# Optimization experiments

Hardware: AMD Instinct MI355X
Metric: run time of the kernel (lower is better)

The kernel has to match this reference:

```python
import jax, jax.numpy as jnp
import numpy as np

EPS = 1e-12  # matches torch F.normalize default


def _l2norm_c(x):
    # normalize along channel dim (axis=1) of [B,C,H,W]
    n = jnp.sqrt(jnp.sum(x * x, axis=1, keepdims=True))
    return x / jnp.maximum(n, EPS)


def setup_inputs() -> dict:
    key = jax.random.key(0)
    ks = jax.random.split(key, 6)
    B, C, H, W = 2, 256, 64, 64
    return {
        "sv": jax.random.normal(ks[0], (B, 1, H, W), dtype=jnp.float32),
        "si": jax.random.normal(ks[1], (B, 1, H, W), dtype=jnp.float32),
        "sf": jax.random.normal(ks[2], (B, 1, H, W), dtype=jnp.float32),
        "dv": jax.random.normal(ks[3], (B, C, H, W), dtype=jnp.float32),
        "di": jax.random.normal(ks[4], (B, C, H, W), dtype=jnp.float32),
        "df": jax.random.normal(ks[5], (B, C, H, W), dtype=jnp.float32),
    }


def reference(sv, si, sf, dv, di, df):
    # keypoint score loss: L1(sf, max(sv, si))
    kp = jnp.mean(jnp.abs(sf - jnp.maximum(sv, si)))
    # descriptor loss: L1(df, (dv+di)/2)
    desc = jnp.mean(jnp.abs(df - (dv + di) * 0.5))
    # match loss (dense): normalize along C, full correlation volumes, L1
    a = _l2norm_c(dv)
    b = _l2norm_c(di)
    c = _l2norm_c(df)
    sim_ab = jnp.einsum('bchw,bcij->bhwij', a, b)  # [B,H,W,H,W]
    sim_ac = jnp.einsum('bchw,bcij->bhwij', a, c)
    match = jnp.mean(jnp.abs(sim_ac - sim_ab))
    return kp + desc + match
```

## Files before the change

### kernel.cpp

```cpp
#include <hip/hip_runtime.h>
#include <hip/hip_bf16.h>
#include <math.h>

#define BB 2
#define CC 256
#define CCP (CC + 2)
#define HWN 4096
#define PT 32
#define TM 128

typedef __attribute__((ext_vector_type(4))) int   intx4;
typedef __attribute__((ext_vector_type(8))) int   intx8;
typedef __attribute__((ext_vector_type(4))) float floatx4;

__device__ __forceinline__ unsigned short f2bf(float f) {
    union { float f; unsigned u; } v; v.f = f;
    unsigned r = v.u + 0x7FFF + ((v.u >> 16) & 1);
    return (unsigned short)(r >> 16);
}

__device__ __forceinline__ float bf2f(unsigned short h) {
    union { unsigned u; float f; } v; v.u = ((unsigned)h) << 16;
    return v.f;
}

__device__ __forceinline__ void load_lds16(const void* g, void* l) {
    __builtin_amdgcn_global_load_lds(
        (const __attribute__((address_space(1))) unsigned int*)g,
        (__attribute__((address_space(3))) unsigned int*)l, 16, 0, 0);
}

__global__ __launch_bounds__(1024) void prep_kernel(
    const float* __restrict__ sv, const float* __restrict__ si,
    const float* __restrict__ sf, const float* __restrict__ dv,
    const float* __restrict__ di, const float* __restrict__ df,
    unsigned char* __restrict__ Af8, unsigned char* __restrict__ Df8,
    float* __restrict__ pk, float* __restrict__ pd)
{
    __shared__ unsigned short lv[PT][CCP];
    __shared__ unsigned short li[PT][CCP];
    __shared__ unsigned short lf[PT][CCP];
    __shared__ float ssq[3][PT];
    __shared__ float inv[3][PT];
    __shared__ float sdesc;

    const int b   = blockIdx.x / (HWN / PT);
    const int p0  = (blockIdx.x % (HWN / PT)) * PT;
    const int tid = threadIdx.x;
    const int tp  = tid & (PT - 1);
    const int cs  = tid >> 5;

    if (tid < 3 * PT) ((float*)ssq)[tid] = 0.0f;
    if (tid == 0) sdesc = 0.0f;
    __syncthreads();

    float sqv = 0.f, sqi = 0.f, sqf = 0.f, descp = 0.f;
    const size_t base = (size_t)b * CC * HWN + p0 + tp;
    #pragma unroll
    for (int j = 0; j < 8; ++j) {
        const int c = cs * 8 + j;
        const size_t idx = base + (size_t)c * HWN;
        const float v = dv[idx], ii = di[idx], ff = df[idx];
        descp += fabsf(ff - 0.5f * (v + ii));
        sqv += v * v; sqi += ii * ii; sqf += ff * ff;
        lv[tp][c] = f2bf(v); li[tp][c] = f2bf(ii); lf[tp][c] = f2bf(ff);
    }
    sqv += __shfl_down(sqv, 32);
    sqi += __shfl_down(sqi, 32);
    sqf += __shfl_down(sqf, 32);
    if ((tid & 63) < 32) {
        atomicAdd(&ssq[0][tp], sqv);
        atomicAdd(&ssq[1][tp], sqi);
        atomicAdd(&ssq[2][tp], sqf);
    }

    #pragma unroll
    for (int off = 32; off > 0; off >>= 1) descp += __shfl_down(descp, off);
    if ((tid & 63) == 0) atomicAdd(&sdesc, descp);

    if (tid < 64) {
        float kpv = 0.f;
        if (tid < PT) {
            const size_t sidx = (size_t)b * HWN + p0 + tid;
            kpv = fabsf(sf[sidx] - fmaxf(sv[sidx], si[sidx]));
        }
        #pragma unroll
        for (int off = 32; off > 0; off >>= 1) kpv += __shfl_down(kpv, off);
        if (tid == 0) pk[blockIdx.x] = kpv;
    }
    __syncthreads();

    if (tid < 3 * PT) {
        const float s = ((float*)ssq)[tid];
        ((float*)inv)[tid] = 1.0f / fmaxf(sqrtf(s), 1e-12f);
    }
    __syncthreads();

    if (tid == 0) pd[blockIdx.x] = sdesc;

    int* Ao = (int*)(Af8 + ((size_t)b * HWN + p0) * CC);
    int* Do = (int*)(Df8 + ((size_t)b * HWN + p0) * CC);
    #pragma unroll
    for (int i = tid; i < PT * CC / 4; i += 1024) {
        const int p = i >> 6, c0 = (i & 63) * 4;
        const float ia = inv[0][p], ib = inv[1][p], ic = inv[2][p];
        float a0 = bf2f(lv[p][c0 + 0]) * ia, a1 = bf2f(lv[p][c0 + 1]) * ia;
        float a2 = bf2f(lv[p][c0 + 2]) * ia, a3 = bf2f(lv[p][c0 + 3]) * ia;
        float d0 = bf2f(lf[p][c0 + 0]) * ic - bf2f(li[p][c0 + 0]) * ib;
        float d1 = bf2f(lf[p][c0 + 1]) * ic - bf2f(li[p][c0 + 1]) * ib;
        float d2 = bf2f(lf[p][c0 + 2]) * ic - bf2f(li[p][c0 + 2]) * ib;
        float d3 = bf2f(lf[p][c0 + 3]) * ic - bf2f(li[p][c0 + 3]) * ib;
        int wa = __builtin_amdgcn_cvt_pk_fp8_f32(a0, a1, 0, false);
        wa     = __builtin_amdgcn_cvt_pk_fp8_f32(a2, a3, wa, true);
        int wd = __builtin_amdgcn_cvt_pk_fp8_f32(d0, d1, 0, false);
        wd     = __builtin_amdgcn_cvt_pk_fp8_f32(d2, d3, wd, true);
        Ao[i] = wa;
        Do[i] = wd;
    }
}

__global__ __launch_bounds__(256) void gemm_abs_kernel(
    const unsigned char* __restrict__ Af8,
    const unsigned char* __restrict__ Df8,
    float* __restrict__ pg)
{
    __shared__ unsigned char lA[TM * CC];
    __shared__ unsigned char lB[TM * CC];

    const int b    = blockIdx.z;
    const int bm   = blockIdx.x * TM;
    const int bn   = blockIdx.y * TM;
    const int tid  = threadIdx.x;
    const int wave = tid >> 6;
    const int lane = tid & 63;
    const int wr   = wave >> 1, wc = wave & 1;

    const unsigned char* Agb = Af8 + (size_t)b * HWN * CC + (size_t)bm * CC;
    const unsigned char* Dgb = Df8 + (size_t)b * HWN * CC + (size_t)bn * CC;

    #pragma unroll
    for (int i = 0; i < 8; ++i) {
        const int r0 = wave * 32 + i * 4;
        const int r  = r0 + (lane >> 4);
        const int cs = (lane & 15) ^ (r & 15);
        const size_t gof = (size_t)r * CC + cs * 16;
        load_lds16(Agb + gof, (char*)lA + r0 * CC);
        load_lds16(Dgb + gof, (char*)lB + r0 * CC);
    }
    __syncthreads();

    floatx4 accf[4][4];
    #pragma unroll
    for (int mi = 0; mi < 4; ++mi)
        #pragma unroll
        for (int ni = 0; ni < 4; ++ni)
            accf[mi][ni] = (floatx4){0.f, 0.f, 0.f, 0.f};

    #pragma unroll
    for (int ks = 0; ks < 2; ++ks) {
        const int cb = ks * 8 + (lane >> 4) * 2;
        intx8 a8[4], b8[4];
        #pragma unroll
        for (int mi = 0; mi < 4; ++mi) {
            const int m = wr * 64 + mi * 16 + (lane & 15);
            const char* pa = (const char*)lA + m * CC;
            intx4 lo = *(const intx4*)(pa + ((cb    ) ^ (m & 15)) * 16);
            intx4 hi = *(const intx4*)(pa + ((cb + 1) ^ (m & 15)) * 16);
            a8[mi] = __builtin_shufflevector(lo, hi, 0, 1, 2, 3, 4, 5, 6, 7);
        }
        #pragma unroll
        for (int ni = 0; ni < 4; ++ni) {
            const int n = wc * 64 + ni * 16 + (lane & 15);
            const char* pb = (const char*)lB + n * CC;
            intx4 lo = *(const intx4*)(pb + ((cb    ) ^ (n & 15)) * 16);
            intx4 hi = *(const intx4*)(pb + ((cb + 1) ^ (n & 15)) * 16);
            b8[ni] = __builtin_shufflevector(lo, hi, 0, 1, 2, 3, 4, 5, 6, 7);
        }
        #pragma unroll
        for (int mi = 0; mi < 4; ++mi)
            #pragma unroll
            for (int ni = 0; ni < 4; ++ni)
                accf[mi][ni] = __builtin_amdgcn_mfma_scale_f32_16x16x128_f8f6f4(
                    a8[mi], b8[ni], accf[mi][ni],
                    0, 0,
                    0, 0x7F7F7F7F,
                    0, 0x7F7F7F7F);
    }

    float s = 0.f;
    #pragma unroll
    for (int mi = 0; mi < 4; ++mi)
        #pragma unroll
        for (int ni = 0; ni < 4; ++ni)
            #pragma unroll
            for (int r = 0; r < 4; ++r)
                s += fabsf(accf[mi][ni][r]);
    #pragma unroll
    for (int off = 32; off > 0; off >>= 1) s += __shfl_down(s, off);
    if (lane == 0) {
        const int flat = blockIdx.x + 32 * (blockIdx.y + 32 * blockIdx.z);
        pg[flat * 4 + wave] = s;
    }
}

__global__ __launch_bounds__(256) void final_kernel(
    const float* __restrict__ pg, const float* __restrict__ pk,
    const float* __restrict__ pd, float* __restrict__ out)
{
    __shared__ float ws[4];
    const int t = threadIdx.x;
    float s = 0.f;
    #pragma unroll
    for (int i = 0; i < 32; ++i)
        s += pg[t + i * 256];
    s *= (1.0f / 33554432.0f);
    s += pk[t] * (1.0f / 8192.0f)
       + pd[t] * (1.0f / 2097152.0f);
    #pragma unroll
    for (int off = 32; off > 0; off >>= 1) s += __shfl_down(s, off);
    if ((t & 63) == 0) ws[t >> 6] = s;
    __syncthreads();
    if (t == 0) out[0] = ws[0] + ws[1] + ws[2] + ws[3];
}

extern "C" void kernel_launch(void* const* d_in, const int* in_sizes, int n_in,
                              void* d_out, int out_size, void* d_ws, size_t ws_size,
                              hipStream_t stream) {
    const float* sv = (const float*)d_in[0];
    const float* si = (const float*)d_in[1];
    const float* sf = (const float*)d_in[2];
    const float* dv = (const float*)d_in[3];
    const float* di = (const float*)d_in[4];
    const float* df = (const float*)d_in[5];

    unsigned char* Af8 = (unsigned char*)d_ws;
    unsigned char* Df8 = Af8 + (size_t)BB * HWN * CC;
    float* pg = (float*)(Df8 + (size_t)BB * HWN * CC);
    float* pk = pg + 8192;
    float* pd = pk + 256;

    prep_kernel<<<dim3(BB * (HWN / PT)), 1024, 0, stream>>>(
        sv, si, sf, dv, di, df, Af8, Df8, pk, pd);
    gemm_abs_kernel<<<dim3(HWN / TM, HWN / TM, BB), 256, 0, stream>>>(
        Af8, Df8, pg);
    final_kernel<<<1, 256, 0, stream>>>(pg, pk, pd, (float*)d_out);
}
```

Before: 96.74 us.

## Vectorize prep loads and fold final reduction into GEMM via last-block counter

Measured after the change: 142.3 us. 47.1% more time.

```diff
diff --git a/kernel.cpp b/kernel.cpp
--- a/kernel.cpp
+++ b/kernel.cpp
@@ -1,5 +1,4 @@
 #include <hip/hip_runtime.h>
-#include <hip/hip_bf16.h>
 #include <math.h>
 
 #define BB 2
@@ -8,6 +7,7 @@
 #define HWN 4096
 #define PT 32
 #define TM 128
+#define GEMM_BLOCKS ((HWN / TM) * (HWN / TM) * BB)
 
 typedef __attribute__((ext_vector_type(4))) int   intx4;
 typedef __attribute__((ext_vector_type(8))) int   intx8;
@@ -35,7 +35,8 @@
     const float* __restrict__ sf, const float* __restrict__ dv,
     const float* __restrict__ di, const float* __restrict__ df,
     unsigned char* __restrict__ Af8, unsigned char* __restrict__ Df8,
-    float* __restrict__ pk, float* __restrict__ pd)
+    float* __restrict__ pk, float* __restrict__ pd,
+    unsigned int* __restrict__ cnt)
 {
     __shared__ unsigned short lv[PT][CCP];
     __shared__ unsigned short li[PT][CCP];
@@ -47,31 +48,54 @@
     const int b   = blockIdx.x / (HWN / PT);
     const int p0  = (blockIdx.x % (HWN / PT)) * PT;
     const int tid = threadIdx.x;
-    const int tp  = tid & (PT - 1);
-    const int cs  = tid >> 5;
-
+    const int p4  = tid & 7;
+    const int cg  = tid >> 3;
+
+    if (blockIdx.x == 0 && tid == 0) cnt[0] = 0u;
     if (tid < 3 * PT) ((float*)ssq)[tid] = 0.0f;
     if (tid == 0) sdesc = 0.0f;
     __syncthreads();
 
-    float sqv = 0.f, sqi = 0.f, sqf = 0.f, descp = 0.f;
-    const size_t base = (size_t)b * CC * HWN + p0 + tp;
-    #pragma unroll
-    for (int j = 0; j < 8; ++j) {
-        const int c = cs * 8 + j;
-        const size_t idx = base + (size_t)c * HWN;
-        const float v = dv[idx], ii = di[idx], ff = df[idx];
-        descp += fabsf(ff - 0.5f * (v + ii));
-        sqv += v * v; sqi += ii * ii; sqf += ff * ff;
-        lv[tp][c] = f2bf(v); li[tp][c] = f2bf(ii); lf[tp][c] = f2bf(ff);
-    }
-    sqv += __shfl_down(sqv, 32);
-    sqi += __shfl_down(sqi, 32);
-    sqf += __shfl_down(sqf, 32);
-    if ((tid & 63) < 32) {
-        atomicAdd(&ssq[0][tp], sqv);
-        atomicAdd(&ssq[1][tp], sqi);
-        atomicAdd(&ssq[2][tp], sqf);
+    float sq[3][4];
+    #pragma unroll
+    for (int j = 0; j < 3; ++j)
+        #pragma unroll
+        for (int k = 0; k < 4; ++k) sq[j][k] = 0.0f;
+    float descp = 0.f;
+
+    #pragma unroll
+    for (int pass = 0; pass < 2; ++pass) {
+        const int c = cg + pass * 128;
+        const size_t idx = (size_t)b * CC * HWN + (size_t)c * HWN + p0 + p4 * 4;
+        const floatx4 v = *(const floatx4*)(dv + idx);
+        const floatx4 w = *(const floatx4*)(di + idx);
+        const floatx4 f = *(const floatx4*)(df + idx);
+        #pragma unroll
+        for (int k = 0; k < 4; ++k) {
+            sq[0][k] += v[k] * v[k];
+            sq[1][k] += w[k] * w[k];
+            sq[2][k] += f[k] * f[k];
+            descp += fabsf(f[k] - 0.5f * (v[k] + w[k]));
+            lv[p4 * 4 + k][c] = f2bf(v[k]);
+            li[p4 * 4 + k][c] = f2bf(w[k]);
+            lf[p4 * 4 + k][c] = f2bf(f[k]);
+        }
+    }
+
+    #pragma unroll
+    for (int m = 8; m < 64; m <<= 1) {
+        #pragma unroll
+        for (int j = 0; j < 3; ++j)
+            #pragma unroll
+            for (int k = 0; k < 4; ++k)
+                sq[j][k] += __shfl_xor(sq[j][k], m);
+    }
+    if ((tid & 63) < 8) {
+        #pragma unroll
+        for (int j = 0; j < 3; ++j)
+            #pragma unroll
+            for (int k = 0; k < 4; ++k)
+                atomicAdd(&ssq[j][p4 * 4 + k], sq[j][k]);
     }
 
     #pragma unroll
@@ -80,12 +104,17 @@
 
     if (tid < 64) {
         float kpv = 0.f;
-        if (tid < PT) {
-            const size_t sidx = (size_t)b * HWN + p0 + tid;
-            kpv = fabsf(sf[sidx] - fmaxf(sv[sidx], si[sidx]));
-        }
-        #pragma unroll
-        for (int off = 32; off > 0; off >>= 1) kpv += __shfl_down(kpv, off);
+        if (tid < 8) {
+            const size_t sidx = (size_t)b * HWN + p0 + tid * 4;
+            const floatx4 a  = *(const floatx4*)(sv + sidx);
+            const floatx4 bq = *(const floatx4*)(si + sidx);
+            const floatx4 cq = *(const floatx4*)(sf + sidx);
+            #pragma unroll
+            for (int k = 0; k < 4; ++k)
+                kpv += fabsf(cq[k] - fmaxf(a[k], bq[k]));
+        }
+        #pragma unroll
+        for (int off = 4; off > 0; off >>= 1) kpv += __shfl_down(kpv, off);
         if (tid == 0) pk[blockIdx.x] = kpv;
     }
     __syncthreads();
@@ -122,10 +151,14 @@
 __global__ __launch_bounds__(256) void gemm_abs_kernel(
     const unsigned char* __restrict__ Af8,
     const unsigned char* __restrict__ Df8,
-    float* __restrict__ pg)
+    float* __restrict__ pg, const float* __restrict__ pk,
+    const float* __restrict__ pd, unsigned int* __restrict__ cnt,
+    float* __restrict__ out)
 {
     __shared__ unsigned char lA[TM * CC];
     __shared__ unsigned char lB[TM * CC];
+    __shared__ float ws4[4];
+    __shared__ unsigned lastf;
 
     const int b    = blockIdx.z;
     const int bm   = blockIdx.x * TM;
@@ -197,30 +230,30 @@
                 s += fabsf(accf[mi][ni][r]);
     #pragma unroll
     for (int off = 32; off > 0; off >>= 1) s += __shfl_down(s, off);
-    if (lane == 0) {
-        const int flat = blockIdx.x + 32 * (blockIdx.y + 32 * blockIdx.z);
-        pg[flat * 4 + wave] = s;
-    }
-}
-
-__global__ __launch_bounds__(256) void final_kernel(
-    const float* __restrict__ pg, const float* __restrict__ pk,
-    const float* __restrict__ pd, float* __restrict__ out)
-{
-    __shared__ float ws[4];
-    const int t = threadIdx.x;
-    float s = 0.f;
-    #pragma unroll
-    for (int i = 0; i < 32; ++i)
-        s += pg[t + i * 256];
-    s *= (1.0f / 33554432.0f);
-    s += pk[t] * (1.0f / 8192.0f)
-       + pd[t] * (1.0f / 2097152.0f);
-    #pragma unroll
-    for (int off = 32; off > 0; off >>= 1) s += __shfl_down(s, off);
-    if ((t & 63) == 0) ws[t >> 6] = s;
-    __syncthreads();
-    if (t == 0) out[0] = ws[0] + ws[1] + ws[2] + ws[3];
+    const int flat = blockIdx.x + 32 * (blockIdx.y + 32 * blockIdx.z);
+    if (lane == 0) pg[flat * 4 + wave] = s;
+
+    __syncthreads();
+    if (tid == 0) {
+        __threadfence();
+        lastf = (atomicAdd(cnt, 1u) == (unsigned)(GEMM_BLOCKS - 1)) ? 1u : 0u;
+    }
+    __syncthreads();
+    if (lastf) {
+        __threadfence();
+        float s2 = 0.f;
+        #pragma unroll
+        for (int i = 0; i < 32; ++i)
+            s2 += pg[tid + i * 256];
+        s2 *= (1.0f / 33554432.0f);
+        s2 += pk[tid] * (1.0f / 8192.0f)
+            + pd[tid] * (1.0f / 2097152.0f);
+        #pragma unroll
+        for (int off = 32; off > 0; off >>= 1) s2 += __shfl_down(s2, off);
+        if ((tid & 63) == 0) ws4[tid >> 6] = s2;
+        __syncthreads();
+        if (tid == 0) out[0] = ws4[0] + ws4[1] + ws4[2] + ws4[3];
+    }
 }
 
 extern "C" void kernel_launch(void* const* d_in, const int* in_sizes, int n_in,
@@ -238,10 +271,10 @@
     float* pg = (float*)(Df8 + (size_t)BB * HWN * CC);
     float* pk = pg + 8192;
     float* pd = pk + 256;
+    unsigned int* cnt = (unsigned int*)(pd + 256);
 
     prep_kernel<<<dim3(BB * (HWN / PT)), 1024, 0, stream>>>(
-        sv, si, sf, dv, di, df, Af8, Df8, pk, pd);
+        sv, si, sf, dv, di, df, Af8, Df8, pk, pd, cnt);
     gemm_abs_kernel<<<dim3(HWN / TM, HWN / TM, BB), 256, 0, stream>>>(
-        Af8, Df8, pg);
-    final_kernel<<<1, 256, 0, stream>>>(pg, pk, pd, (float*)d_out);
-}
+        Af8, Df8, pg, pk, pd, cnt, (float*)d_out);
+}
```
